# Kernel optimization log

Measured on AMD Instinct MI355X. Metric: run time of the kernel, lower is better.

## Reference

```python
import jax, jax.numpy as jnp
import numpy as np

D_MODEL = 256
N_LAYERS = 4
D_STATE = 16
D_CONV = 4
D_INNER = 2 * D_MODEL          # expand=2
DT_RANK = (D_MODEL + 15) // 16  # 'auto' -> ceil(d_model/16) = 16
NUM_CLASSES = 10
BATCH = 4
HW = 32


def setup_inputs() -> dict:
    key = jax.random.key(0)
    ks = jax.random.split(key, 16)
    std = 0.02
    inp = {}
    inp["x"] = jax.random.normal(ks[0], (BATCH, 3, HW, HW), dtype=jnp.float32)
    inp["input_proj_w"] = std * jax.random.normal(ks[1], (D_MODEL, 3), dtype=jnp.float32)
    inp["input_proj_b"] = jnp.zeros((D_MODEL,), jnp.float32)
    inp["in_proj_w"] = std * jax.random.normal(ks[2], (N_LAYERS, 2 * D_INNER, D_MODEL), dtype=jnp.float32)
    inp["conv_w"] = std * jax.random.normal(ks[3], (N_LAYERS, D_INNER, D_CONV), dtype=jnp.float32)
    inp["conv_b"] = jnp.zeros((N_LAYERS, D_INNER), jnp.float32)
    inp["x_proj_w"] = std * jax.random.normal(ks[4], (N_LAYERS, DT_RANK + 2 * D_STATE, D_INNER), dtype=jnp.float32)
    inp["dt_proj_w"] = std * jax.random.normal(ks[5], (N_LAYERS, D_INNER, DT_RANK), dtype=jnp.float32)
    # dt bias ~ inverse-softplus of small dt values (Mamba-style init)
    inp["dt_proj_b"] = jnp.log(jnp.expm1(0.01 * jnp.ones((N_LAYERS, D_INNER), jnp.float32)))
    # A_log init: log(1..d_state) per channel (Mamba S4D-real init)
    a = jnp.log(jnp.arange(1, D_STATE + 1, dtype=jnp.float32))
    inp["A_log"] = jnp.broadcast_to(a, (N_LAYERS, D_INNER, D_STATE)).copy()
    inp["D_skip"] = jnp.ones((N_LAYERS, D_INNER), jnp.float32)
    inp["out_proj_w"] = std * jax.random.normal(ks[6], (N_LAYERS, D_MODEL, D_INNER), dtype=jnp.float32)
    inp["ln_w"] = jnp.ones((N_LAYERS, D_MODEL), jnp.float32)
    inp["ln_b"] = jnp.zeros((N_LAYERS, D_MODEL), jnp.float32)
    inp["fn_w"] = jnp.ones((D_MODEL,), jnp.float32)
    inp["fn_b"] = jnp.zeros((D_MODEL,), jnp.float32)
    inp["cls_w"] = std * jax.random.normal(ks[7], (NUM_CLASSES, D_MODEL), dtype=jnp.float32)
    inp["cls_b"] = jnp.zeros((NUM_CLASSES,), jnp.float32)
    return inp


def _layer_norm(x, w, b, eps=1e-5):
    mu = jnp.mean(x, axis=-1, keepdims=True)
    var = jnp.mean(jnp.square(x - mu), axis=-1, keepdims=True)
    return (x - mu) * jax.lax.rsqrt(var + eps) * w + b


def _mamba_block(x, in_w, cw, cb, xp_w, dt_w, dt_b, A_log, D_skip, out_w):
    B_, L, _ = x.shape
    xz = jnp.einsum('bld,ed->ble', x, in_w)            # [B,L,2*Din]
    xh, z = jnp.split(xz, 2, axis=-1)                  # [B,L,Din] each
    # depthwise causal conv1d (kernel D_CONV, left pad D_CONV-1)
    xp = jnp.pad(xh, ((0, 0), (D_CONV - 1, 0), (0, 0)))
    conv = cb + sum(xp[:, k:k + L, :] * cw[:, k] for k in range(D_CONV))
    xh = jax.nn.silu(conv)
    x_dbl = jnp.einsum('bld,ed->ble', xh, xp_w)        # [B,L,dt_rank+2N]
    dt, Bm, Cm = jnp.split(x_dbl, [DT_RANK, DT_RANK + D_STATE], axis=-1)
    delta = jax.nn.softplus(jnp.einsum('blr,dr->bld', dt, dt_w) + dt_b)  # [B,L,Din]
    A = -jnp.exp(A_log)                                # [Din,N]
    deltaA = jnp.exp(delta[..., None] * A)             # [B,L,Din,N]
    deltaBu = delta[..., None] * Bm[:, :, None, :] * xh[..., None]       # [B,L,Din,N]

    def step(h, inputs):
        dA_t, dBu_t, C_t = inputs
        h = dA_t * h + dBu_t                           # [B,Din,N]
        y = jnp.einsum('bdn,bn->bd', h, C_t)
        return h, y

    h0 = jnp.zeros((B_, D_INNER, D_STATE), x.dtype)
    _, ys = jax.lax.scan(step, h0, (deltaA.transpose(1, 0, 2, 3),
                                    deltaBu.transpose(1, 0, 2, 3),
                                    Cm.transpose(1, 0, 2)))
    y = ys.transpose(1, 0, 2) + xh * D_skip            # [B,L,Din]
    y = y * jax.nn.silu(z)
    return jnp.einsum('bld,od->blo', y, out_w)         # [B,L,Dmodel]


def reference(x, input_proj_w, input_proj_b, in_proj_w, conv_w, conv_b,
              x_proj_w, dt_proj_w, dt_proj_b, A_log, D_skip, out_proj_w,
              ln_w, ln_b, fn_w, fn_b, cls_w, cls_b):
    B_ = x.shape[0]
    seq = x.transpose(0, 2, 3, 1).reshape(B_, -1, 3)   # [B, H*W, 3]
    h = jnp.einsum('blc,dc->bld', seq, input_proj_w) + input_proj_b
    for i in range(N_LAYERS):
        res = h
        h = _layer_norm(h, ln_w[i], ln_b[i])
        h = _mamba_block(h, in_proj_w[i], conv_w[i], conv_b[i], x_proj_w[i],
                         dt_proj_w[i], dt_proj_b[i], A_log[i], D_skip[i], out_proj_w[i])
        h = h + res  # dropout is identity (p=0 / eval)
    h = jnp.mean(h, axis=1)                            # [B, Dmodel]
    h = _layer_norm(h, fn_w, fn_b)
    return h @ cls_w.T + cls_b                         # [B, num_classes]
```

## Files before the change

kernel.cpp:

```cpp
#include <hip/hip_runtime.h>
#include <math.h>

#define B_ 4
#define L_ 1024
#define DM 256
#define DIN 512
#define NST 16
#define DTR 16
#define CHK 64
#define CT (L_ / CHK)

typedef short short8 __attribute__((ext_vector_type(8)));
typedef float float4v __attribute__((ext_vector_type(4)));

__device__ __forceinline__ float softplusf(float x) {
    return (x > 20.f) ? x : log1pf(__expf(x));
}
__device__ __forceinline__ float siluf(float x) {
    return x / (1.f + __expf(-x));
}
__device__ __forceinline__ unsigned short f2bf(float f) {
    unsigned int u = __float_as_uint(f);
    u = (u + 0x7fffu + ((u >> 16) & 1u)) >> 16;
    return (unsigned short)u;
}

__device__ __forceinline__ void block_reduce2(float& a, float& q) {
    #pragma unroll
    for (int off = 32; off > 0; off >>= 1) {
        a += __shfl_down(a, off);
        q += __shfl_down(q, off);
    }
    __shared__ float sa[4], sq[4];
    int lane = threadIdx.x & 63, w = threadIdx.x >> 6;
    if (lane == 0) { sa[w] = a; sq[w] = q; }
    __syncthreads();
    a = sa[0] + sa[1] + sa[2] + sa[3];
    q = sq[0] + sq[1] + sq[2] + sq[3];
}

__global__ __launch_bounds__(256) void prologue_kernel(
    const float* __restrict__ inw, int na, const float* __restrict__ xpw, int nb,
    const float* __restrict__ opw, int nc,
    unsigned short* __restrict__ oa, unsigned short* __restrict__ ob,
    unsigned short* __restrict__ oc, int nconv,
    const float* __restrict__ x, const float* __restrict__ ipw,
    const float* __restrict__ ipb, float* __restrict__ h0)
{
    if ((int)blockIdx.x < nconv) {
        int i = blockIdx.x * 256 + threadIdx.x;
        if (i < na) { oa[i] = f2bf(inw[i]); return; }
        int j = i - na;
        if (j < nb) { ob[j] = f2bf(xpw[j]); return; }
        int k = j - nb;
        if (k < nc) oc[k] = f2bf(opw[k]);
        return;
    }
    int idx = (blockIdx.x - nconv) * 256 + threadIdx.x;
    int d = idx & (DM - 1);
    int bl = idx >> 8;
    int l = bl & (L_ - 1);
    int b = bl >> 10;
    const float* xb = x + (size_t)b * 3 * L_;
    float acc = ipb[d];
    acc = fmaf(xb[0 * L_ + l], ipw[d * 3 + 0], acc);
    acc = fmaf(xb[1 * L_ + l], ipw[d * 3 + 1], acc);
    acc = fmaf(xb[2 * L_ + l], ipw[d * 3 + 2], acc);
    h0[idx] = acc;
}

__global__ __launch_bounds__(256) void gemm_in_ln(
    const float* __restrict__ A, const unsigned short* __restrict__ W,
    const float* __restrict__ lw, const float* __restrict__ lb,
    float* __restrict__ C, int N)
{
    __shared__ unsigned short As[64][264];
    __shared__ unsigned short Ws[64][72];
    const int tid = threadIdx.x;
    const int wave = tid >> 6;
    const int lane = tid & 63;
    const int m_l = lane & 15;
    const int q = lane >> 4;
    const int m0 = blockIdx.y * 64;
    const int n0 = blockIdx.x * 64;

    {
        const int rg = lane >> 4;
        const int c4 = lane & 15;
        #pragma unroll
        for (int p = 0; p < 4; ++p) {
            int r = p * 16 + wave * 4 + rg;
            const float* ap = A + (size_t)(m0 + r) * DM;
            float4 v[4];
            float s = 0.f, qq = 0.f;
            #pragma unroll
            for (int i = 0; i < 4; ++i) {
                v[i] = *(const float4*)(ap + i * 64 + c4 * 4);
                s  += v[i].x + v[i].y + v[i].z + v[i].w;
                qq += v[i].x * v[i].x + v[i].y * v[i].y
                    + v[i].z * v[i].z + v[i].w * v[i].w;
            }
            s += __shfl_xor(s, 1); qq += __shfl_xor(qq, 1);
            s += __shfl_xor(s, 2); qq += __shfl_xor(qq, 2);
            s += __shfl_xor(s, 4); qq += __shfl_xor(qq, 4);
            s += __shfl_xor(s, 8); qq += __shfl_xor(qq, 8);
            float mu = s * (1.f / DM);
            float var = qq * (1.f / DM) - mu * mu;
            float rs = rsqrtf(var + 1e-5f);
            #pragma unroll
            for (int i = 0; i < 4; ++i) {
                int col = i * 64 + c4 * 4;
                float4 wv = *(const float4*)(lw + col);
                float4 bv = *(const float4*)(lb + col);
                unsigned short* dst = &As[r][col];
                dst[0] = f2bf((v[i].x - mu) * rs * wv.x + bv.x);
                dst[1] = f2bf((v[i].y - mu) * rs * wv.y + bv.y);
                dst[2] = f2bf((v[i].z - mu) * rs * wv.z + bv.z);
                dst[3] = f2bf((v[i].w - mu) * rs * wv.w + bv.w);
            }
        }
    }
    __syncthreads();

    const int sr = tid >> 3;
    const int sc = (tid & 7) * 8;
    float4v acc[4];
    #pragma unroll
    for (int j = 0; j < 4; ++j) acc[j] = (float4v)(0.f);

    for (int k0 = 0; k0 < DM; k0 += 64) {
        *(short8*)&Ws[sr][sc]      = *(const short8*)(W + (size_t)(n0 + sr) * DM + k0 + sc);
        *(short8*)&Ws[sr + 32][sc] = *(const short8*)(W + (size_t)(n0 + sr + 32) * DM + k0 + sc);
        __syncthreads();
        #pragma unroll
        for (int kk = 0; kk < 64; kk += 32) {
            short8 a = *(const short8*)&As[wave * 16 + m_l][k0 + kk + q * 8];
            #pragma unroll
            for (int j4 = 0; j4 < 4; ++j4) {
                short8 b = *(const short8*)&Ws[j4 * 16 + m_l][kk + q * 8];
                acc[j4] = __builtin_amdgcn_mfma_f32_16x16x32_bf16(a, b, acc[j4], 0, 0, 0);
            }
        }
        __syncthreads();
    }
    #pragma unroll
    for (int j4 = 0; j4 < 4; ++j4) {
        int n = n0 + j4 * 16 + m_l;
        #pragma unroll
        for (int reg = 0; reg < 4; ++reg) {
            int m = m0 + wave * 16 + q * 4 + reg;
            C[(size_t)m * N + n] = acc[j4][reg];
        }
    }
}

__global__ __launch_bounds__(512) void conv_xproj_summary(
    const float* __restrict__ xz, const float* __restrict__ cw,
    const float* __restrict__ cb, const unsigned short* __restrict__ W,
    const float* __restrict__ A_log, const float* __restrict__ dt_w,
    const float* __restrict__ dt_b,
    float* __restrict__ dbc, float* __restrict__ S, float* __restrict__ H)
{
    __shared__ unsigned short As[CT][520];
    __shared__ float Dbc[CT][64];
    const int tid = threadIdx.x;
    const int d = tid;
    const int c = blockIdx.x;
    const int b = blockIdx.y;
    const int l0 = c * CT;

    float xcr[CT];
    {
        const float w0 = cw[d * 4 + 0], w1 = cw[d * 4 + 1];
        const float w2 = cw[d * 4 + 2], w3 = cw[d * 4 + 3];
        const float cbv = cb[d];
        const float* xp = xz + ((size_t)(b * L_ + l0)) * (2 * DIN) + d;
        float x0 = 0.f, x1 = 0.f, x2 = 0.f;
        if (l0 >= 3) {
            x0 = xp[(ptrdiff_t)(-3) * (2 * DIN)];
            x1 = xp[(ptrdiff_t)(-2) * (2 * DIN)];
            x2 = xp[(ptrdiff_t)(-1) * (2 * DIN)];
        }
        #pragma unroll
        for (int t = 0; t < CT; ++t) {
            float x3 = xp[(size_t)t * (2 * DIN)];
            float a = fmaf(x0, w0, cbv);
            a = fmaf(x1, w1, a);
            a = fmaf(x2, w2, a);
            a = fmaf(x3, w3, a);
            float v = siluf(a);
            xcr[t] = v;
            As[t][d] = f2bf(v);
            x0 = x1; x1 = x2; x2 = x3;
        }
    }
    __syncthreads();

    {
        const int wave = tid >> 6;
        const int lane = tid & 63;
        const int m_l = lane & 15;
        const int q = lane >> 4;
        if (wave < 3) {
            float4v acc = (float4v)(0.f);
            for (int k0 = 0; k0 < DIN; k0 += 32) {
                short8 a  = *(const short8*)&As[m_l][k0 + q * 8];
                short8 bf = *(const short8*)(W + (size_t)(wave * 16 + m_l) * DIN + k0 + q * 8);
                acc = __builtin_amdgcn_mfma_f32_16x16x32_bf16(a, bf, acc, 0, 0, 0);
            }
            #pragma unroll
            for (int reg = 0; reg < 4; ++reg)
                Dbc[q * 4 + reg][wave * 16 + m_l] = acc[reg];
        }
    }
    __syncthreads();

    for (int i = tid; i < CT * 48; i += 512) {
        int t = i / 48, col = i - t * 48;
        dbc[((size_t)(b * L_ + l0 + t)) * 48 + col] = Dbc[t][col];
    }

    float A[NST], tw[DTR];
    #pragma unroll
    for (int j = 0; j < NST; ++j) A[j] = -__expf(A_log[d * NST + j]);
    #pragma unroll
    for (int r = 0; r < DTR; ++r) tw[r] = dt_w[d * DTR + r];
    const float tb = dt_b[d];
    float h[NST];
    #pragma unroll
    for (int j = 0; j < NST; ++j) h[j] = 0.f;
    float ssum = 0.f;
    #pragma unroll 4
    for (int t = 0; t < CT; ++t) {
        float acc = tb;
        #pragma unroll
        for (int r = 0; r < DTR; ++r) acc = fmaf(Dbc[t][r], tw[r], acc);
        float dlt = softplusf(acc);
        float t0 = dlt * xcr[t];
        ssum += dlt;
        #pragma unroll
        for (int j = 0; j < NST; ++j) {
            float dA = __expf(A[j] * dlt);
            h[j] = fmaf(dA, h[j], t0 * Dbc[t][DTR + j]);
        }
    }
    S[((size_t)b * CHK + c) * DIN + d] = ssum;
    float* Hp = H + (((size_t)b * CHK + c) * NST) * DIN + d;
    #pragma unroll
    for (int j = 0; j < NST; ++j)
        Hp[(size_t)j * DIN] = h[j];
}

__global__ __launch_bounds__(256) void scan_prefix_kernel(
    const float* __restrict__ S, float* __restrict__ H,
    const float* __restrict__ A_log)
{
    int idx = blockIdx.x * 256 + threadIdx.x;
    int d = idx & (DIN - 1);
    int n = (idx >> 9) & (NST - 1);
    int b = idx >> 13;
    float A = -__expf(A_log[d * NST + n]);
    float hprev = 0.f;
    const float* Sp = S + (size_t)b * CHK * DIN + d;
    float* Hp = H + (((size_t)b * CHK) * NST + n) * DIN + d;
    for (int c = 0; c < CHK; ++c) {
        float Hc = Hp[(size_t)c * NST * DIN];
        float Sc = Sp[(size_t)c * DIN];
        Hp[(size_t)c * NST * DIN] = hprev;
        hprev = fmaf(__expf(A * Sc), hprev, Hc);
    }
}

__global__ __launch_bounds__(512) void scan_apply_out(
    const float* __restrict__ dbc, const float* __restrict__ xz,
    const float* __restrict__ cw, const float* __restrict__ cb,
    const float* __restrict__ A_log, const float* __restrict__ dt_w,
    const float* __restrict__ dt_b, const float* __restrict__ Dskip,
    const float* __restrict__ H, const unsigned short* __restrict__ Wout,
    float* __restrict__ hbuf)
{
    __shared__ unsigned short Ys[CT][520];
    const int tid = threadIdx.x;
    const int d = tid;
    const int c = blockIdx.x;
    const int b = blockIdx.y;
    const int l0 = c * CT;

    {
        float A[NST], tw[DTR];
        #pragma unroll
        for (int j = 0; j < NST; ++j) A[j] = -__expf(A_log[d * NST + j]);
        #pragma unroll
        for (int r = 0; r < DTR; ++r) tw[r] = dt_w[d * DTR + r];
        const float tb = dt_b[d];
        const float Dsk = Dskip[d];
        const float* bc = dbc + ((size_t)(b * L_ + l0)) * 48;
        const float* xp = xz  + ((size_t)(b * L_ + l0)) * (2 * DIN) + d;
        const float* zp = xp + DIN;

        const float w0 = cw[d * 4 + 0], w1 = cw[d * 4 + 1];
        const float w2 = cw[d * 4 + 2], w3 = cw[d * 4 + 3];
        const float cbv = cb[d];
        float x0 = 0.f, x1 = 0.f, x2 = 0.f;
        if (l0 >= 3) {
            x0 = xp[(ptrdiff_t)(-3) * (2 * DIN)];
            x1 = xp[(ptrdiff_t)(-2) * (2 * DIN)];
            x2 = xp[(ptrdiff_t)(-1) * (2 * DIN)];
        }

        float h[NST];
        const float* Hp = H + (((size_t)b * CHK + c) * NST) * DIN + d;
        #pragma unroll
        for (int j = 0; j < NST; ++j) h[j] = Hp[(size_t)j * DIN];

        #pragma unroll 4
        for (int t = 0; t < CT; ++t) {
            float x3 = xp[(size_t)t * (2 * DIN)];
            float ca = fmaf(x0, w0, cbv);
            ca = fmaf(x1, w1, ca);
            ca = fmaf(x2, w2, ca);
            ca = fmaf(x3, w3, ca);
            float xcv = siluf(ca);
            x0 = x1; x1 = x2; x2 = x3;

            const float* br = bc + t * 48;
            float acc = tb;
            #pragma unroll
            for (int r = 0; r < DTR; ++r) acc = fmaf(br[r], tw[r], acc);
            float dlt = softplusf(acc);
            float zv  = zp[(size_t)t * (2 * DIN)];
            float t0 = dlt * xcv;
            float p = 0.f;
            #pragma unroll
            for (int j = 0; j < NST; ++j) {
                float dA = __expf(A[j] * dlt);
                h[j] = fmaf(dA, h[j], t0 * br[DTR + j]);
                p = fmaf(h[j], br[DTR + NST + j], p);
            }
            Ys[t][d] = f2bf((p + xcv * Dsk) * siluf(zv));
        }
    }
    __syncthreads();

    {
        const int wave = tid >> 6;
        const int lane = tid & 63;
        const int m_l = lane & 15;
        const int q = lane >> 4;
        #pragma unroll
        for (int nt = 0; nt < 2; ++nt) {
            const int n0 = (wave * 2 + nt) * 16;
            float4v acc = (float4v)(0.f);
            for (int k0 = 0; k0 < DIN; k0 += 32) {
                short8 a = *(const short8*)&Ys[m_l][k0 + q * 8];
                short8 w = *(const short8*)(Wout + (size_t)(n0 + m_l) * DIN + k0 + q * 8);
                acc = __builtin_amdgcn_mfma_f32_16x16x32_bf16(a, w, acc, 0, 0, 0);
            }
            #pragma unroll
            for (int reg = 0; reg < 4; ++reg) {
                int row = q * 4 + reg;
                hbuf[((size_t)(b * L_ + l0 + row)) * DM + n0 + m_l] += acc[reg];
            }
        }
    }
}

__global__ __launch_bounds__(256) void head_partial_kernel(
    const float* __restrict__ h, float* __restrict__ partial)
{
    int b = blockIdx.x >> 4, ch = blockIdx.x & 15, t = threadIdx.x;
    const float* hp = h + ((size_t)(b * L_ + ch * 64)) * DM + t;
    float s = 0.f;
    #pragma unroll 8
    for (int l = 0; l < 64; ++l) s += hp[(size_t)l * DM];
    partial[(size_t)blockIdx.x * DM + t] = s;
}

__global__ __launch_bounds__(256) void head_final_kernel(
    const float* __restrict__ partial, const float* __restrict__ fn_w,
    const float* __restrict__ fn_b, const float* __restrict__ cls_w,
    const float* __restrict__ cls_b, float* __restrict__ out)
{
    int b = blockIdx.x, t = threadIdx.x;
    const float* pp = partial + (size_t)b * 16 * DM + t;
    float s = 0.f;
    #pragma unroll
    for (int c = 0; c < 16; ++c) s += pp[(size_t)c * DM];
    s *= (1.f / L_);
    float a = s, q = s * s;
    block_reduce2(a, q);
    float mu = a * (1.f / DM);
    float var = q * (1.f / DM) - mu * mu;
    float v = (s - mu) * rsqrtf(var + 1e-5f) * fn_w[t] + fn_b[t];
    __shared__ float pooled[DM];
    pooled[t] = v;
    __syncthreads();
    if (t < 10) {
        float acc = cls_b[t];
        for (int d2 = 0; d2 < DM; ++d2)
            acc = fmaf(pooled[d2], cls_w[t * DM + d2], acc);
        out[b * 10 + t] = acc;
    }
}

extern "C" void kernel_launch(void* const* d_in, const int* in_sizes, int n_in,
                              void* d_out, int out_size, void* d_ws, size_t ws_size,
                              hipStream_t stream)
{
    const float* x    = (const float*)d_in[0];
    const float* ipw  = (const float*)d_in[1];
    const float* ipb  = (const float*)d_in[2];
    const float* inw  = (const float*)d_in[3];
    const float* cw   = (const float*)d_in[4];
    const float* cb   = (const float*)d_in[5];
    const float* xpw  = (const float*)d_in[6];
    const float* dtw  = (const float*)d_in[7];
    const float* dtb  = (const float*)d_in[8];
    const float* alog = (const float*)d_in[9];
    const float* dsk  = (const float*)d_in[10];
    const float* opw  = (const float*)d_in[11];
    const float* lnw  = (const float*)d_in[12];
    const float* lnb  = (const float*)d_in[13];
    const float* fnw  = (const float*)d_in[14];
    const float* fnb  = (const float*)d_in[15];
    const float* clw  = (const float*)d_in[16];
    const float* clb  = (const float*)d_in[17];

    float* ws     = (float*)d_ws;
    float* hbuf   = ws;
    float* xzbuf  = hbuf   + (size_t)B_ * L_ * DM;
    float* dbcbuf = xzbuf  + (size_t)B_ * L_ * 2 * DIN;
    float* Sbuf   = dbcbuf + (size_t)B_ * L_ * 48;
    float* Hbuf   = Sbuf   + (size_t)B_ * CHK * DIN;
    float* tail   = Hbuf   + (size_t)B_ * CHK * NST * DIN;
    unsigned short* inw16 = (unsigned short*)tail;
    unsigned short* xpw16 = inw16 + (size_t)4 * 1024 * DM;
    unsigned short* opw16 = xpw16 + (size_t)4 * 48 * DIN;
    float* partial = (float*)(opw16 + (size_t)4 * DM * DIN);

    const int BL = B_ * L_;
    const int NIN = 4 * 1024 * DM, NXP = 4 * 48 * DIN, NOP = 4 * DM * DIN;
    const int NCONV = (NIN + NXP + NOP + 255) / 256;

    prologue_kernel<<<NCONV + BL * DM / 256, 256, 0, stream>>>(
        inw, NIN, xpw, NXP, opw, NOP, inw16, xpw16, opw16, NCONV,
        x, ipw, ipb, hbuf);

    for (int i = 0; i < 4; ++i) {
        gemm_in_ln<<<dim3(2 * DIN / 64, BL / 64), 256, 0, stream>>>(
            hbuf, inw16 + (size_t)i * 1024 * DM, lnw + i * DM, lnb + i * DM,
            xzbuf, 2 * DIN);
        conv_xproj_summary<<<dim3(CHK, B_), 512, 0, stream>>>(
            xzbuf, cw + i * DIN * 4, cb + i * DIN,
            xpw16 + (size_t)i * 48 * DIN, alog + i * DIN * NST,
            dtw + i * DIN * DTR, dtb + i * DIN, dbcbuf, Sbuf, Hbuf);
        scan_prefix_kernel<<<B_ * NST * DIN / 256, 256, 0, stream>>>(
            Sbuf, Hbuf, alog + i * DIN * NST);
        scan_apply_out<<<dim3(CHK, B_), 512, 0, stream>>>(
            dbcbuf, xzbuf, cw + i * DIN * 4, cb + i * DIN,
            alog + i * DIN * NST, dtw + i * DIN * DTR, dtb + i * DIN,
            dsk + i * DIN, Hbuf, opw16 + (size_t)i * DM * DIN, hbuf);
    }

    head_partial_kernel<<<B_ * 16, 256, 0, stream>>>(hbuf, partial);
    head_final_kernel<<<B_, 256, 0, stream>>>(partial, fnw, fnb, clw, clb,
                                              (float*)d_out);
}
```

Before: 385.6 us.

## Move LayerNorm into producer epilogues and fuse mean-pool into last scan kernel

The LayerNorm that used to run at the start of the in-projection GEMM now runs in the epilogue of the previous stage (prologue or scan_apply_out), which writes a bf16 normalized copy. The GEMM becomes a plain bf16 GEMM that streams K tiles for both operands. The residual add is staged in shared memory and seeded into the MFMA accumulators. The last layer writes per-chunk row sums directly, which removes the separate head_partial kernel. This saves fp32 activation reads and a kernel launch, at the cost of more shared memory and extra epilogue work in scan_apply_out.

```diff
diff --git a/kernel.cpp b/kernel.cpp
--- a/kernel.cpp
+++ b/kernel.cpp
@@ -45,7 +45,9 @@
     unsigned short* __restrict__ oa, unsigned short* __restrict__ ob,
     unsigned short* __restrict__ oc, int nconv,
     const float* __restrict__ x, const float* __restrict__ ipw,
-    const float* __restrict__ ipb, float* __restrict__ h0)
+    const float* __restrict__ ipb, const float* __restrict__ lw0,
+    const float* __restrict__ lb0, float* __restrict__ h0,
+    unsigned short* __restrict__ ln16)
 {
     if ((int)blockIdx.x < nconv) {
         int i = blockIdx.x * 256 + threadIdx.x;
@@ -56,25 +58,30 @@
         if (k < nc) oc[k] = f2bf(opw[k]);
         return;
     }
-    int idx = (blockIdx.x - nconv) * 256 + threadIdx.x;
-    int d = idx & (DM - 1);
-    int bl = idx >> 8;
-    int l = bl & (L_ - 1);
-    int b = bl >> 10;
+    int row = blockIdx.x - nconv;
+    int l = row & (L_ - 1);
+    int b = row >> 10;
+    int d = threadIdx.x;
     const float* xb = x + (size_t)b * 3 * L_;
+    float x0 = xb[l], x1 = xb[L_ + l], x2 = xb[2 * L_ + l];
     float acc = ipb[d];
-    acc = fmaf(xb[0 * L_ + l], ipw[d * 3 + 0], acc);
-    acc = fmaf(xb[1 * L_ + l], ipw[d * 3 + 1], acc);
-    acc = fmaf(xb[2 * L_ + l], ipw[d * 3 + 2], acc);
-    h0[idx] = acc;
-}
-
-__global__ __launch_bounds__(256) void gemm_in_ln(
-    const float* __restrict__ A, const unsigned short* __restrict__ W,
-    const float* __restrict__ lw, const float* __restrict__ lb,
-    float* __restrict__ C, int N)
-{
-    __shared__ unsigned short As[64][264];
+    acc = fmaf(x0, ipw[d * 3 + 0], acc);
+    acc = fmaf(x1, ipw[d * 3 + 1], acc);
+    acc = fmaf(x2, ipw[d * 3 + 2], acc);
+    float a = acc, q = acc * acc;
+    block_reduce2(a, q);
+    float mu = a * (1.f / DM);
+    float var = q * (1.f / DM) - mu * mu;
+    float rs = rsqrtf(var + 1e-5f);
+    h0[(size_t)row * DM + d] = acc;
+    ln16[(size_t)row * DM + d] = f2bf((acc - mu) * rs * lw0[d] + lb0[d]);
+}
+
+__global__ __launch_bounds__(256) void gemm_bt_bf16(
+    const unsigned short* __restrict__ A, const unsigned short* __restrict__ W,
+    float* __restrict__ C, int M, int N, int K, int lda)
+{
+    __shared__ unsigned short As[64][72];
     __shared__ unsigned short Ws[64][72];
     const int tid = threadIdx.x;
     const int wave = tid >> 6;
@@ -83,62 +90,26 @@
     const int q = lane >> 4;
     const int m0 = blockIdx.y * 64;
     const int n0 = blockIdx.x * 64;
-
-    {
-        const int rg = lane >> 4;
-        const int c4 = lane & 15;
-        #pragma unroll
-        for (int p = 0; p < 4; ++p) {
-            int r = p * 16 + wave * 4 + rg;
-            const float* ap = A + (size_t)(m0 + r) * DM;
-            float4 v[4];
-            float s = 0.f, qq = 0.f;
-            #pragma unroll
-            for (int i = 0; i < 4; ++i) {
-                v[i] = *(const float4*)(ap + i * 64 + c4 * 4);
-                s  += v[i].x + v[i].y + v[i].z + v[i].w;
-                qq += v[i].x * v[i].x + v[i].y * v[i].y
-                    + v[i].z * v[i].z + v[i].w * v[i].w;
-            }
-            s += __shfl_xor(s, 1); qq += __shfl_xor(qq, 1);
-            s += __shfl_xor(s, 2); qq += __shfl_xor(qq, 2);
-            s += __shfl_xor(s, 4); qq += __shfl_xor(qq, 4);
-            s += __shfl_xor(s, 8); qq += __shfl_xor(qq, 8);
-            float mu = s * (1.f / DM);
-            float var = qq * (1.f / DM) - mu * mu;
-            float rs = rsqrtf(var + 1e-5f);
-            #pragma unroll
-            for (int i = 0; i < 4; ++i) {
-                int col = i * 64 + c4 * 4;
-                float4 wv = *(const float4*)(lw + col);
-                float4 bv = *(const float4*)(lb + col);
-                unsigned short* dst = &As[r][col];
-                dst[0] = f2bf((v[i].x - mu) * rs * wv.x + bv.x);
-                dst[1] = f2bf((v[i].y - mu) * rs * wv.y + bv.y);
-                dst[2] = f2bf((v[i].z - mu) * rs * wv.z + bv.z);
-                dst[3] = f2bf((v[i].w - mu) * rs * wv.w + bv.w);
-            }
-        }
-    }
-    __syncthreads();
-
     const int sr = tid >> 3;
     const int sc = (tid & 7) * 8;
+
     float4v acc[4];
     #pragma unroll
     for (int j = 0; j < 4; ++j) acc[j] = (float4v)(0.f);
 
-    for (int k0 = 0; k0 < DM; k0 += 64) {
-        *(short8*)&Ws[sr][sc]      = *(const short8*)(W + (size_t)(n0 + sr) * DM + k0 + sc);
-        *(short8*)&Ws[sr + 32][sc] = *(const short8*)(W + (size_t)(n0 + sr + 32) * DM + k0 + sc);
+    for (int k0 = 0; k0 < K; k0 += 64) {
+        *(short8*)&As[sr][sc]      = *(const short8*)(A + (size_t)(m0 + sr) * lda + k0 + sc);
+        *(short8*)&As[sr + 32][sc] = *(const short8*)(A + (size_t)(m0 + sr + 32) * lda + k0 + sc);
+        *(short8*)&Ws[sr][sc]      = *(const short8*)(W + (size_t)(n0 + sr) * K + k0 + sc);
+        *(short8*)&Ws[sr + 32][sc] = *(const short8*)(W + (size_t)(n0 + sr + 32) * K + k0 + sc);
         __syncthreads();
         #pragma unroll
         for (int kk = 0; kk < 64; kk += 32) {
-            short8 a = *(const short8*)&As[wave * 16 + m_l][k0 + kk + q * 8];
+            short8 a = *(const short8*)&As[wave * 16 + m_l][kk + q * 8];
             #pragma unroll
             for (int j4 = 0; j4 < 4; ++j4) {
-                short8 b = *(const short8*)&Ws[j4 * 16 + m_l][kk + q * 8];
-                acc[j4] = __builtin_amdgcn_mfma_f32_16x16x32_bf16(a, b, acc[j4], 0, 0, 0);
+                short8 bf = *(const short8*)&Ws[j4 * 16 + m_l][kk + q * 8];
+                acc[j4] = __builtin_amdgcn_mfma_f32_16x16x32_bf16(a, bf, acc[j4], 0, 0, 0);
             }
         }
         __syncthreads();
@@ -277,9 +248,12 @@
     const float* __restrict__ A_log, const float* __restrict__ dt_w,
     const float* __restrict__ dt_b, const float* __restrict__ Dskip,
     const float* __restrict__ H, const unsigned short* __restrict__ Wout,
-    float* __restrict__ hbuf)
+    float* __restrict__ hbuf, const float* __restrict__ nlw,
+    const float* __restrict__ nlb, unsigned short* __restrict__ ln16,
+    float* __restrict__ chunkpartial, int last)
 {
     __shared__ unsigned short Ys[CT][520];
+    __shared__ float hrow[CT][264];
     const int tid = threadIdx.x;
     const int d = tid;
     const int c = blockIdx.x;
@@ -343,6 +317,15 @@
     __syncthreads();
 
     {
+        const int row = tid >> 5;
+        const int col0 = (tid & 31) * 8;
+        const float* hg = hbuf + ((size_t)(b * L_ + l0 + row)) * DM + col0;
+        *(float4*)&hrow[row][col0]     = *(const float4*)hg;
+        *(float4*)&hrow[row][col0 + 4] = *(const float4*)(hg + 4);
+    }
+    __syncthreads();
+
+    {
         const int wave = tid >> 6;
         const int lane = tid & 63;
         const int m_l = lane & 15;
@@ -350,42 +333,69 @@
         #pragma unroll
         for (int nt = 0; nt < 2; ++nt) {
             const int n0 = (wave * 2 + nt) * 16;
-            float4v acc = (float4v)(0.f);
+            float4v acc;
+            #pragma unroll
+            for (int reg = 0; reg < 4; ++reg)
+                acc[reg] = hrow[q * 4 + reg][n0 + m_l];
             for (int k0 = 0; k0 < DIN; k0 += 32) {
                 short8 a = *(const short8*)&Ys[m_l][k0 + q * 8];
                 short8 w = *(const short8*)(Wout + (size_t)(n0 + m_l) * DIN + k0 + q * 8);
                 acc = __builtin_amdgcn_mfma_f32_16x16x32_bf16(a, w, acc, 0, 0, 0);
             }
             #pragma unroll
-            for (int reg = 0; reg < 4; ++reg) {
-                int row = q * 4 + reg;
-                hbuf[((size_t)(b * L_ + l0 + row)) * DM + n0 + m_l] += acc[reg];
-            }
-        }
-    }
-}
-
-__global__ __launch_bounds__(256) void head_partial_kernel(
-    const float* __restrict__ h, float* __restrict__ partial)
-{
-    int b = blockIdx.x >> 4, ch = blockIdx.x & 15, t = threadIdx.x;
-    const float* hp = h + ((size_t)(b * L_ + ch * 64)) * DM + t;
+            for (int reg = 0; reg < 4; ++reg)
+                hrow[q * 4 + reg][n0 + m_l] = acc[reg];
+        }
+    }
+    __syncthreads();
+
+    if (!last) {
+        const int row = tid >> 5;
+        const int c32 = tid & 31;
+        const int col0 = c32 * 8;
+        float v[8];
+        float s = 0.f, qq = 0.f;
+        #pragma unroll
+        for (int i = 0; i < 8; ++i) {
+            v[i] = hrow[row][col0 + i];
+            s += v[i];
+            qq += v[i] * v[i];
+        }
+        s += __shfl_xor(s, 1);  qq += __shfl_xor(qq, 1);
+        s += __shfl_xor(s, 2);  qq += __shfl_xor(qq, 2);
+        s += __shfl_xor(s, 4);  qq += __shfl_xor(qq, 4);
+        s += __shfl_xor(s, 8);  qq += __shfl_xor(qq, 8);
+        s += __shfl_xor(s, 16); qq += __shfl_xor(qq, 16);
+        float mu = s * (1.f / DM);
+        float var = qq * (1.f / DM) - mu * mu;
+        float rs = rsqrtf(var + 1e-5f);
+        float* hg = hbuf + ((size_t)(b * L_ + l0 + row)) * DM + col0;
+        *(float4*)hg       = make_float4(v[0], v[1], v[2], v[3]);
+        *(float4*)(hg + 4) = make_float4(v[4], v[5], v[6], v[7]);
+        unsigned short* lo = ln16 + ((size_t)(b * L_ + l0 + row)) * DM + col0;
+        #pragma unroll
+        for (int i = 0; i < 8; ++i)
+            lo[i] = f2bf((v[i] - mu) * rs * nlw[col0 + i] + nlb[col0 + i]);
+    } else {
+        if (tid < DM) {
+            float s = 0.f;
+            #pragma unroll
+            for (int t = 0; t < CT; ++t) s += hrow[t][tid];
+            chunkpartial[((size_t)(b * CHK + c)) * DM + tid] = s;
+        }
+    }
+}
+
+__global__ __launch_bounds__(256) void head_final_kernel(
+    const float* __restrict__ chunkpartial, const float* __restrict__ fn_w,
+    const float* __restrict__ fn_b, const float* __restrict__ cls_w,
+    const float* __restrict__ cls_b, float* __restrict__ out)
+{
+    int b = blockIdx.x, t = threadIdx.x;
+    const float* pp = chunkpartial + (size_t)b * CHK * DM + t;
     float s = 0.f;
     #pragma unroll 8
-    for (int l = 0; l < 64; ++l) s += hp[(size_t)l * DM];
-    partial[(size_t)blockIdx.x * DM + t] = s;
-}
-
-__global__ __launch_bounds__(256) void head_final_kernel(
-    const float* __restrict__ partial, const float* __restrict__ fn_w,
-    const float* __restrict__ fn_b, const float* __restrict__ cls_w,
-    const float* __restrict__ cls_b, float* __restrict__ out)
-{
-    int b = blockIdx.x, t = threadIdx.x;
-    const float* pp = partial + (size_t)b * 16 * DM + t;
-    float s = 0.f;
-    #pragma unroll
-    for (int c = 0; c < 16; ++c) s += pp[(size_t)c * DM];
+    for (int c = 0; c < CHK; ++c) s += pp[(size_t)c * DM];
     s *= (1.f / L_);
     float a = s, q = s * s;
     block_reduce2(a, q);
@@ -432,37 +442,40 @@
     float* dbcbuf = xzbuf  + (size_t)B_ * L_ * 2 * DIN;
     float* Sbuf   = dbcbuf + (size_t)B_ * L_ * 48;
     float* Hbuf   = Sbuf   + (size_t)B_ * CHK * DIN;
-    float* tail   = Hbuf   + (size_t)B_ * CHK * NST * DIN;
-    unsigned short* inw16 = (unsigned short*)tail;
+    float* cpart  = Hbuf   + (size_t)B_ * CHK * NST * DIN;
+    float* tail   = cpart  + (size_t)B_ * CHK * DM;
+    unsigned short* ln16  = (unsigned short*)tail;
+    unsigned short* inw16 = ln16  + (size_t)B_ * L_ * DM;
     unsigned short* xpw16 = inw16 + (size_t)4 * 1024 * DM;
     unsigned short* opw16 = xpw16 + (size_t)4 * 48 * DIN;
-    float* partial = (float*)(opw16 + (size_t)4 * DM * DIN);
 
     const int BL = B_ * L_;
     const int NIN = 4 * 1024 * DM, NXP = 4 * 48 * DIN, NOP = 4 * DM * DIN;
     const int NCONV = (NIN + NXP + NOP + 255) / 256;
 
-    prologue_kernel<<<NCONV + BL * DM / 256, 256, 0, stream>>>(
+    prologue_kernel<<<NCONV + BL, 256, 0, stream>>>(
         inw, NIN, xpw, NXP, opw, NOP, inw16, xpw16, opw16, NCONV,
-        x, ipw, ipb, hbuf);
+        x, ipw, ipb, lnw, lnb, hbuf, ln16);
 
     for (int i = 0; i < 4; ++i) {
-        gemm_in_ln<<<dim3(2 * DIN / 64, BL / 64), 256, 0, stream>>>(
-            hbuf, inw16 + (size_t)i * 1024 * DM, lnw + i * DM, lnb + i * DM,
-            xzbuf, 2 * DIN);
+        gemm_bt_bf16<<<dim3(2 * DIN / 64, BL / 64), 256, 0, stream>>>(
+            ln16, inw16 + (size_t)i * 1024 * DM, xzbuf, BL, 2 * DIN, DM, DM);
         conv_xproj_summary<<<dim3(CHK, B_), 512, 0, stream>>>(
             xzbuf, cw + i * DIN * 4, cb + i * DIN,
             xpw16 + (size_t)i * 48 * DIN, alog + i * DIN * NST,
             dtw + i * DIN * DTR, dtb + i * DIN, dbcbuf, Sbuf, Hbuf);
         scan_prefix_kernel<<<B_ * NST * DIN / 256, 256, 0, stream>>>(
             Sbuf, Hbuf, alog + i * DIN * NST);
+        int last = (i == 3);
+        const float* nlw = lnw + (last ? 0 : (i + 1) * DM);
+        const float* nlb = lnb + (last ? 0 : (i + 1) * DM);
         scan_apply_out<<<dim3(CHK, B_), 512, 0, stream>>>(
             dbcbuf, xzbuf, cw + i * DIN * 4, cb + i * DIN,
             alog + i * DIN * NST, dtw + i * DIN * DTR, dtb + i * DIN,
-            dsk + i * DIN, Hbuf, opw16 + (size_t)i * DM * DIN, hbuf);
-    }
-
-    head_partial_kernel<<<B_ * 16, 256, 0, stream>>>(hbuf, partial);
-    head_final_kernel<<<B_, 256, 0, stream>>>(partial, fnw, fnb, clw, clb,
+            dsk + i * DIN, Hbuf, opw16 + (size_t)i * DM * DIN, hbuf,
+            nlw, nlb, ln16, cpart, last);
+    }
+
+    head_final_kernel<<<B_, 256, 0, stream>>>(cpart, fnw, fnb, clw, clb,
                                               (float*)d_out);
 }
```

Result: no change. 385.6 us (-0.0%).
